# Performance work log

Measured on AMD Instinct MI355X. Metric: run time of the kernel, lower is better.

The kernel has to match this reference:

```python
import jax, jax.numpy as jnp
import numpy as np

N_E = 8192
E_DIM = 256
BETA = 0.25


def setup_inputs() -> dict:
    key = jax.random.key(0)
    k1, k2 = jax.random.split(key)
    z = jax.random.normal(k1, (16, E_DIM, 32, 32), dtype=jnp.float32)
    # matches torch init: uniform(-1/n_e, 1/n_e)
    emb_w = jax.random.uniform(k2, (N_E, E_DIM), dtype=jnp.float32,
                               minval=-1.0 / N_E, maxval=1.0 / N_E)
    return {"z": z, "emb_w": emb_w}


def reference(z, emb_w):
    B, C, H, W = z.shape
    zt = jnp.transpose(z, (0, 2, 3, 1))          # b h w c
    zf = zt.reshape(-1, C)                        # [N, e_dim]
    # d[n, k] = ||zf_n||^2 + ||e_k||^2 - 2 zf_n . e_k
    d = (jnp.sum(zf * zf, axis=1, keepdims=True)
         + jnp.sum(emb_w * emb_w, axis=1)
         - 2.0 * jnp.einsum('bd,nd->bn', zf, emb_w))
    idx = jnp.argmin(d, axis=1)                   # [N]
    z_q = emb_w[idx].reshape(zt.shape)            # b h w c
    sg = jax.lax.stop_gradient
    # legacy=True loss
    loss = jnp.mean((sg(z_q) - zt) ** 2) + BETA * jnp.mean((z_q - sg(zt)) ** 2)
    # straight-through estimator
    z_q_st = zt + sg(z_q - zt)
    z_q_out = jnp.transpose(z_q_st, (0, 3, 1, 2))  # b c h w
    return z_q_out, loss, idx.reshape(B, H, W)
```

## Files before the change

### kernel.cpp

```cpp
#include <hip/hip_runtime.h>
#include <math.h>

typedef unsigned int uint;
typedef unsigned short ushort;
typedef unsigned long long u64;
typedef __attribute__((ext_vector_type(8))) short short8;
typedef __attribute__((ext_vector_type(4))) float f32x4;

#define WS_ZT   0ull
#define WS_ZPK  16777216ull
#define WS_EPK  25165824ull
#define WS_SUMZ 29360128ull
#define WS_GMAX 29425664ull
#define WS_CMAX 46202880ull
#define WS_BEST 50397184ull
#define WS_LOSS 50528256ull

#define DOT_MARGIN 1.5e-4f

__device__ __forceinline__ ushort f2bf(float f) {
  uint b = __float_as_uint(f);
  b += 0x7fffu + ((b >> 16) & 1u);
  return (ushort)(b >> 16);
}
__device__ __forceinline__ uint ford(float f) {
  uint b = __float_as_uint(f);
  return (b & 0x80000000u) ? ~b : (b | 0x80000000u);
}
__device__ __forceinline__ void gload_lds16(const void* g, void* l) {
  __builtin_amdgcn_global_load_lds(
      (const __attribute__((address_space(1))) unsigned int*)g,
      (__attribute__((address_space(3))) unsigned int*)l, 16, 0, 0);
}

__global__ __launch_bounds__(256) void prep_all(const float* __restrict__ z,
                                                const float* __restrict__ emb,
                                                float* __restrict__ zt,
                                                ushort* __restrict__ zpk,
                                                ushort* __restrict__ epk,
                                                float* __restrict__ sumz) {
  __shared__ float tile[64][65];
  const int bidg = blockIdx.x;
  const int t = threadIdx.x;
  if (bidg < 1024) {
    const int bid = bidg;
    const int kt = bid & 3, hwt = (bid >> 2) & 15, b = bid >> 6;
    const int lane = t & 63, grp = t >> 6;
    const float* src = z + b * 262144 + (kt * 64) * 1024 + hwt * 64;
    for (int kk = grp; kk < 64; kk += 4)
      tile[kk][lane] = src[kk * 1024 + lane];
    __syncthreads();
    for (int rr = grp; rr < 64; rr += 4) {
      const int n = b * 1024 + hwt * 64 + rr;
      zt[n * 256 + kt * 64 + lane] = tile[lane][rr];
    }
    for (int u = t; u < 512; u += 256) {
      const int n_loc = u & 63, kg = u >> 6;
      const int n = b * 1024 + hwt * 64 + n_loc;
      const int k0 = kt * 64 + kg * 8;
      short8 s;
#pragma unroll
      for (int j = 0; j < 8; ++j) s[j] = (short)f2bf(tile[kg * 8 + j][n_loc]);
      *(short8*)(zpk + (size_t)(n >> 4) * 4096 + (k0 >> 5) * 512 +
                 ((k0 >> 3) & 3) * 128 + (n & 15) * 8) = s;
    }
  } else if (bidg < 2048) {
    const int u = (bidg - 1024) * 256 + t;
    const int c = u >> 5, k0 = (u & 31) * 8;
    const float4 v0 = *(const float4*)(emb + c * 256 + k0);
    const float4 v1 = *(const float4*)(emb + c * 256 + k0 + 4);
    short8 s;
    s[0] = (short)f2bf(v0.x); s[1] = (short)f2bf(v0.y);
    s[2] = (short)f2bf(v0.z); s[3] = (short)f2bf(v0.w);
    s[4] = (short)f2bf(v1.x); s[5] = (short)f2bf(v1.y);
    s[6] = (short)f2bf(v1.z); s[7] = (short)f2bf(v1.w);
    *(short8*)(epk + (size_t)(c >> 4) * 4096 + (k0 >> 5) * 512 +
               ((k0 >> 3) & 3) * 128 + (c & 15) * 8) = s;
  } else {
    const int n = ((bidg - 2048) << 8) + t;
    const int b = n >> 10, hw = n & 1023;
    const float* zb = z + b * 262144 + hw;
    float s = 0.f;
#pragma unroll 8
    for (int c = 0; c < 256; ++c) { const float v = zb[c << 10]; s += v * v; }
    sumz[n] = s;
  }
}

__global__ __launch_bounds__(256) void gemm_screen(const ushort* __restrict__ zpk,
                                                   const ushort* __restrict__ epk,
                                                   uint* __restrict__ gmax16,
                                                   ushort* __restrict__ cmax,
                                                   int boff) {
  __shared__ ushort Cs[16384];
  const int t = threadIdx.x;
  const int w = t >> 6, lane = t & 63;
  const int bid = blockIdx.x + boff;
  const int x = bid & 7, y = bid >> 3;
  const int yyv = y & 15;
  const int colb = yyv * 8 + x;
  const int rowg = y >> 4;
  const int n0 = rowg << 10;
  const int m16 = lane & 15, q = lane >> 4;

#pragma unroll
  for (int f2 = 0; f2 < 8; ++f2) {
    const int f = w * 8 + f2;
    gload_lds16(epk + (size_t)colb * 16384 + f * 512 + lane * 8, (char*)Cs + f * 1024);
  }

  const ushort* zw = zpk + ((size_t)(n0 >> 4) + w * 4) * 4096 + lane * 8;

  short8 zf[32][4];
#pragma unroll
  for (int v = 0; v < 3; ++v)
#pragma unroll
    for (int jr = 0; jr < 4; ++jr)
      zf[v][jr] = *(const short8*)(zw + ((size_t)((v >> 3) * 16 + jr)) * 4096 +
                                   (v & 7) * 512);
  __syncthreads();

#pragma unroll
  for (int strip = 0; strip < 4; ++strip) {
    const int rbase = n0 + strip * 256 + w * 64;
    f32x4 acc[4][4];
#pragma unroll
    for (int i = 0; i < 4; ++i)
#pragma unroll
      for (int j = 0; j < 4; ++j) acc[i][j] = {0.f, 0.f, 0.f, 0.f};

#pragma unroll
    for (int s32 = 0; s32 < 8; ++s32) {
      const int v = strip * 8 + s32;
      if (v + 3 < 32) {
        const int u = v + 3;
#pragma unroll
        for (int jr = 0; jr < 4; ++jr)
          zf[u][jr] = *(const short8*)(zw + ((size_t)((u >> 3) * 16 + jr)) * 4096 +
                                       (u & 7) * 512);
      }
      short8 cv[4];
#pragma unroll
      for (int ic = 0; ic < 4; ++ic)
        cv[ic] = *(const short8*)&Cs[(size_t)(ic * 8 + s32) * 512 + lane * 8];
#pragma unroll
      for (int ic = 0; ic < 4; ++ic)
#pragma unroll
        for (int jr = 0; jr < 4; ++jr)
          acc[ic][jr] = __builtin_amdgcn_mfma_f32_16x16x32_bf16(cv[ic], zf[v][jr],
                                                                acc[ic][jr], 0, 0, 0);
    }

#pragma unroll
    for (int jr = 0; jr < 4; ++jr) {
      float g16[4];
      float pm = -INFINITY;
#pragma unroll
      for (int ic = 0; ic < 4; ++ic) {
        float m = fmaxf(fmaxf(acc[ic][jr][0], acc[ic][jr][1]),
                        fmaxf(acc[ic][jr][2], acc[ic][jr][3]));
        m = fmaxf(m, __shfl_xor(m, 16, 64));
        const float o = __shfl_xor(m, 32, 64);
        const float g = fmaxf(m, o);
        g16[ic] = g;
        pm = fmaxf(pm, g);
      }
      const int row = rbase + jr * 16 + m16;
      const uint pa = (uint)f2bf(g16[0]) | ((uint)f2bf(g16[1]) << 16);
      const uint pb = (uint)f2bf(g16[2]) | ((uint)f2bf(g16[3]) << 16);
      if (q < 2)
        gmax16[(size_t)row * 256 + x * 32 + yyv * 2 + q] = (q == 0) ? pa : pb;
      if (q == 2)
        cmax[(size_t)row * 128 + x * 16 + yyv] = f2bf(pm);
    }
  }
}

__global__ __launch_bounds__(256) void select_rescore(const uint* __restrict__ gmax16,
                                                      const ushort* __restrict__ cmax,
                                                      const float* __restrict__ zt,
                                                      const float* __restrict__ emb,
                                                      const float* __restrict__ sumz,
                                                      u64* __restrict__ best) {
  const int t = threadIdx.x, w = t >> 6, lane = t & 63;
  const int n = (blockIdx.x << 2) + w;
  __shared__ float zrow[4][256];
  __shared__ ushort cands[4][32];
  ((float4*)zrow[w])[lane] = ((const float4*)(zt + (size_t)n * 256))[lane];

  const uint cu = ((const uint*)cmax)[(size_t)n * 64 + lane];
  const float c0 = __uint_as_float(cu << 16);
  const float c1 = __uint_as_float(cu & 0xffff0000u);
  float m = fmaxf(c0, c1);
#pragma unroll
  for (int off = 1; off < 64; off <<= 1) m = fmaxf(m, __shfl_xor(m, off, 64));
  const float thr = m - DOT_MARGIN;

  u64 m0 = __ballot(c0 >= thr);
  u64 m1 = __ballot(c1 >= thr);
  int nc = 0;
  while (m0 | m1) {
    int colp;
    if (m0) { const int s = __ffsll(m0) - 1; m0 &= m0 - 1; colp = s * 2; }
    else    { const int s = __ffsll(m1) - 1; m1 &= m1 - 1; colp = s * 2 + 1; }
    const int xx = colp >> 4, yy = colp & 15;
    const uint ua = gmax16[(size_t)n * 256 + xx * 32 + yy * 2];
    const uint ub = gmax16[(size_t)n * 256 + xx * 32 + yy * 2 + 1];
    const int gb = (yy * 8 + xx) * 4;
    const float f0 = __uint_as_float(ua << 16);
    const float f1 = __uint_as_float(ua & 0xffff0000u);
    const float f2 = __uint_as_float(ub << 16);
    const float f3 = __uint_as_float(ub & 0xffff0000u);
    if (f0 >= thr && nc < 32) { cands[w][nc] = (ushort)(gb + 0); ++nc; }
    if (f1 >= thr && nc < 32) { cands[w][nc] = (ushort)(gb + 1); ++nc; }
    if (f2 >= thr && nc < 32) { cands[w][nc] = (ushort)(gb + 2); ++nc; }
    if (f3 >= thr && nc < 32) { cands[w][nc] = (ushort)(gb + 3); ++nc; }
  }

  const int K = nc;
  const float sz = sumz[n];
  u64 bk = ~0ull;
  for (int id = lane; id < K * 16; id += 64) {
    const int g = cands[w][id >> 4];
    const int c = (g >> 2) * 64 + (g & 3) * 16 + (id & 15);
    const float4* ea = (const float4*)(emb + c * 256);
    const float4* za = (const float4*)zrow[w];
    float sdot = 0.f, se = 0.f;
#pragma unroll 8
    for (int k = 0; k < 64; ++k) {
      const float4 a = za[k], e = ea[k];
      sdot = fmaf(a.x, e.x, sdot); sdot = fmaf(a.y, e.y, sdot);
      sdot = fmaf(a.z, e.z, sdot); sdot = fmaf(a.w, e.w, sdot);
      se = fmaf(e.x, e.x, se); se = fmaf(e.y, e.y, se);
      se = fmaf(e.z, e.z, se); se = fmaf(e.w, e.w, se);
    }
    const float d = (sz + se) - 2.f * sdot;
    const u64 key = ((u64)ford(d) << 32) | (uint)c;
    if (key < bk) bk = key;
  }
#pragma unroll
  for (int off = 1; off < 64; off <<= 1) {
    const u64 o = (((u64)(uint)__shfl_xor((int)(bk >> 32), off, 64)) << 32) |
                  (uint)__shfl_xor((int)(bk & 0xffffffffu), off, 64);
    if (o < bk) bk = o;
  }
  if (lane == 0) best[n] = bk;
}

__global__ __launch_bounds__(256) void gather_kernel(const float* __restrict__ z,
                                                     const float* __restrict__ emb,
                                                     const u64* __restrict__ best,
                                                     float* __restrict__ out,
                                                     double* __restrict__ loss_acc,
                                                     uint* __restrict__ done) {
  const int t = threadIdx.x;
  const int n0 = blockIdx.x << 6;
  const int n = n0 + (t & 63);
  const int idx = (int)(best[n] & 0xffffffffull);
  const int b_i = n >> 10, hw = n & 1023;
  const int c0 = t >> 6;
  const float* zb = z + b_i * 262144 + hw;
  float* ob = out + b_i * 262144 + hw;
  const float* eb = emb + idx * 256;
  float lsum = 0.f;
#pragma unroll 4
  for (int c = c0; c < 256; c += 4) {
    const float ev = eb[c];
    const float zv = zb[c << 10];
    ob[c << 10] = ev;
    const float d = ev - zv;
    lsum += d * d;
  }
  if (c0 == 0) out[4194305 + n] = (float)idx;
#pragma unroll
  for (int off = 32; off; off >>= 1) lsum += __shfl_down(lsum, off, 64);
  __shared__ double wsum[4];
  if ((t & 63) == 0) wsum[t >> 6] = (double)lsum;
  __syncthreads();
  if (t == 0) {
    atomicAdd(loss_acc, wsum[0] + wsum[1] + wsum[2] + wsum[3]);
    __threadfence();
    if (atomicAdd(done, 1u) == 255u) {
      __threadfence();
      out[4194304] = (float)(1.25 * (*(volatile double*)loss_acc) / 4194304.0);
    }
  }
}

extern "C" void kernel_launch(void* const* d_in, const int* in_sizes, int n_in,
                              void* d_out, int out_size, void* d_ws, size_t ws_size,
                              hipStream_t stream) {
  const float* z = (const float*)d_in[0];
  const float* emb = (const float*)d_in[1];
  float* out = (float*)d_out;
  char* ws = (char*)d_ws;
  float* zt = (float*)(ws + WS_ZT);
  ushort* zpk = (ushort*)(ws + WS_ZPK);
  ushort* epk = (ushort*)(ws + WS_EPK);
  float* sumz = (float*)(ws + WS_SUMZ);
  uint* gmax16 = (uint*)(ws + WS_GMAX);
  ushort* cmax = (ushort*)(ws + WS_CMAX);
  u64* best = (u64*)(ws + WS_BEST);
  double* loss_acc = (double*)(ws + WS_LOSS);
  uint* done = (uint*)(ws + WS_LOSS + 8);

  hipMemsetAsync(ws + WS_LOSS, 0, 16, stream);
  prep_all<<<2112, 256, 0, stream>>>(z, emb, zt, zpk, epk, sumz);
  gemm_screen<<<1024, 256, 0, stream>>>(zpk, epk, gmax16, cmax, 0);
  gemm_screen<<<1024, 256, 0, stream>>>(zpk, epk, gmax16, cmax, 1024);
  select_rescore<<<4096, 256, 0, stream>>>(gmax16, cmax, zt, emb, sumz, best);
  gather_kernel<<<256, 256, 0, stream>>>(z, emb, best, out, loss_acc, done);
}
```

Before: 265.1 us.

## Refine screening to 8-code groups and drop transposed fp32 z copy

The gemm screen now stores per-row maxima for groups of 8 codes instead of 16, so rescoring evaluates fewer candidate codes in exact fp32. The 16 MB transposed z copy is removed; select_rescore gathers each z row from the original strided layout instead. The best index is stored as a 32-bit uint. This trades a doubled gmax buffer write and strided z reads against less prep traffic and fewer fp32 dot products.

```diff
diff --git a/kernel.cpp b/kernel.cpp
--- a/kernel.cpp
+++ b/kernel.cpp
@@ -7,14 +7,13 @@
 typedef __attribute__((ext_vector_type(8))) short short8;
 typedef __attribute__((ext_vector_type(4))) float f32x4;
 
-#define WS_ZT   0ull
-#define WS_ZPK  16777216ull
-#define WS_EPK  25165824ull
-#define WS_SUMZ 29360128ull
-#define WS_GMAX 29425664ull
+#define WS_ZPK  0ull
+#define WS_EPK  8388608ull
+#define WS_SUMZ 12582912ull
+#define WS_GMAX 12648448ull
 #define WS_CMAX 46202880ull
 #define WS_BEST 50397184ull
-#define WS_LOSS 50528256ull
+#define WS_LOSS 50462720ull
 
 #define DOT_MARGIN 1.5e-4f
 
@@ -35,7 +34,6 @@
 
 __global__ __launch_bounds__(256) void prep_all(const float* __restrict__ z,
                                                 const float* __restrict__ emb,
-                                                float* __restrict__ zt,
                                                 ushort* __restrict__ zpk,
                                                 ushort* __restrict__ epk,
                                                 float* __restrict__ sumz) {
@@ -50,10 +48,6 @@
     for (int kk = grp; kk < 64; kk += 4)
       tile[kk][lane] = src[kk * 1024 + lane];
     __syncthreads();
-    for (int rr = grp; rr < 64; rr += 4) {
-      const int n = b * 1024 + hwt * 64 + rr;
-      zt[n * 256 + kt * 64 + lane] = tile[lane][rr];
-    }
     for (int u = t; u < 512; u += 256) {
       const int n_loc = u & 63, kg = u >> 6;
       const int n = b * 1024 + hwt * 64 + n_loc;
@@ -89,7 +83,7 @@
 
 __global__ __launch_bounds__(256) void gemm_screen(const ushort* __restrict__ zpk,
                                                    const ushort* __restrict__ epk,
-                                                   uint* __restrict__ gmax16,
+                                                   uint* __restrict__ gmax,
                                                    ushort* __restrict__ cmax,
                                                    int boff) {
   __shared__ ushort Cs[16384];
@@ -102,6 +96,7 @@
   const int rowg = y >> 4;
   const int n0 = rowg << 10;
   const int m16 = lane & 15, q = lane >> 4;
+  const int cix = x * 64 + yyv * 4 + q;
 
 #pragma unroll
   for (int f2 = 0; f2 < 8; ++f2) {
@@ -153,7 +148,7 @@
 
 #pragma unroll
     for (int jr = 0; jr < 4; ++jr) {
-      float g16[4];
+      uint pk[4];
       float pm = -INFINITY;
 #pragma unroll
       for (int ic = 0; ic < 4; ++ic) {
@@ -161,32 +156,33 @@
                         fmaxf(acc[ic][jr][2], acc[ic][jr][3]));
         m = fmaxf(m, __shfl_xor(m, 16, 64));
         const float o = __shfl_xor(m, 32, 64);
-        const float g = fmaxf(m, o);
-        g16[ic] = g;
-        pm = fmaxf(pm, g);
+        pm = fmaxf(pm, fmaxf(m, o));
+        const float glo = (q & 2) ? o : m;
+        const float ghi = (q & 2) ? m : o;
+        pk[ic] = (uint)f2bf(glo) | ((uint)f2bf(ghi) << 16);
       }
+      const uint sv = (q == 0) ? pk[0] : (q == 1) ? pk[1] : (q == 2) ? pk[2] : pk[3];
       const int row = rbase + jr * 16 + m16;
-      const uint pa = (uint)f2bf(g16[0]) | ((uint)f2bf(g16[1]) << 16);
-      const uint pb = (uint)f2bf(g16[2]) | ((uint)f2bf(g16[3]) << 16);
-      if (q < 2)
-        gmax16[(size_t)row * 256 + x * 32 + yyv * 2 + q] = (q == 0) ? pa : pb;
-      if (q == 2)
-        cmax[(size_t)row * 128 + x * 16 + yyv] = f2bf(pm);
-    }
-  }
-}
-
-__global__ __launch_bounds__(256) void select_rescore(const uint* __restrict__ gmax16,
+      gmax[(size_t)row * 512 + cix] = sv;
+      if (q == 0) cmax[(size_t)row * 128 + x * 16 + yyv] = f2bf(pm);
+    }
+  }
+}
+
+__global__ __launch_bounds__(256) void select_rescore(const uint* __restrict__ gmax,
                                                       const ushort* __restrict__ cmax,
-                                                      const float* __restrict__ zt,
+                                                      const float* __restrict__ z,
                                                       const float* __restrict__ emb,
                                                       const float* __restrict__ sumz,
-                                                      u64* __restrict__ best) {
+                                                      uint* __restrict__ bestI) {
   const int t = threadIdx.x, w = t >> 6, lane = t & 63;
   const int n = (blockIdx.x << 2) + w;
   __shared__ float zrow[4][256];
-  __shared__ ushort cands[4][32];
-  ((float4*)zrow[w])[lane] = ((const float4*)(zt + (size_t)n * 256))[lane];
+  __shared__ ushort hits[4][64];
+  const int b_i = n >> 10, hw = n & 1023;
+  const float* zb = z + b_i * 262144 + hw;
+#pragma unroll
+  for (int j = 0; j < 4; ++j) zrow[w][lane + j * 64] = zb[(lane + j * 64) << 10];
 
   const uint cu = ((const uint*)cmax)[(size_t)n * 64 + lane];
   const float c0 = __uint_as_float(cu << 16);
@@ -198,31 +194,29 @@
 
   u64 m0 = __ballot(c0 >= thr);
   u64 m1 = __ballot(c1 >= thr);
-  int nc = 0;
+  int nh = 0;
   while (m0 | m1) {
-    int colp;
-    if (m0) { const int s = __ffsll(m0) - 1; m0 &= m0 - 1; colp = s * 2; }
-    else    { const int s = __ffsll(m1) - 1; m1 &= m1 - 1; colp = s * 2 + 1; }
-    const int xx = colp >> 4, yy = colp & 15;
-    const uint ua = gmax16[(size_t)n * 256 + xx * 32 + yy * 2];
-    const uint ub = gmax16[(size_t)n * 256 + xx * 32 + yy * 2 + 1];
-    const int gb = (yy * 8 + xx) * 4;
-    const float f0 = __uint_as_float(ua << 16);
-    const float f1 = __uint_as_float(ua & 0xffff0000u);
-    const float f2 = __uint_as_float(ub << 16);
-    const float f3 = __uint_as_float(ub & 0xffff0000u);
-    if (f0 >= thr && nc < 32) { cands[w][nc] = (ushort)(gb + 0); ++nc; }
-    if (f1 >= thr && nc < 32) { cands[w][nc] = (ushort)(gb + 1); ++nc; }
-    if (f2 >= thr && nc < 32) { cands[w][nc] = (ushort)(gb + 2); ++nc; }
-    if (f3 >= thr && nc < 32) { cands[w][nc] = (ushort)(gb + 3); ++nc; }
-  }
-
-  const int K = nc;
+    int p;
+    if (m0) { const int s = (int)__builtin_ctzll(m0); m0 &= m0 - 1; p = s * 2; }
+    else    { const int s = (int)__builtin_ctzll(m1); m1 &= m1 - 1; p = s * 2 + 1; }
+    const int xx = p >> 4, yy = p & 15;
+    const int cb = (yy * 8 + xx) * 64;
+    const uint4 fw = *(const uint4*)(gmax + (size_t)n * 512 + xx * 64 + yy * 4);
+    const uint fq[4] = {fw.x, fw.y, fw.z, fw.w};
+#pragma unroll
+    for (int qq = 0; qq < 4; ++qq) {
+      if (__uint_as_float(fq[qq] << 16) >= thr && nh < 64)
+        hits[w][nh++] = (ushort)(cb + qq * 16);
+      if (__uint_as_float(fq[qq] & 0xffff0000u) >= thr && nh < 64)
+        hits[w][nh++] = (ushort)(cb + qq * 16 + 8);
+    }
+  }
+  __threadfence_block();
+  const int K = nh;
   const float sz = sumz[n];
   u64 bk = ~0ull;
-  for (int id = lane; id < K * 16; id += 64) {
-    const int g = cands[w][id >> 4];
-    const int c = (g >> 2) * 64 + (g & 3) * 16 + (id & 15);
+  for (int id = lane; id < K * 8; id += 64) {
+    const int c = hits[w][id >> 3] + (id & 7);
     const float4* ea = (const float4*)(emb + c * 256);
     const float4* za = (const float4*)zrow[w];
     float sdot = 0.f, se = 0.f;
@@ -244,19 +238,19 @@
                   (uint)__shfl_xor((int)(bk & 0xffffffffu), off, 64);
     if (o < bk) bk = o;
   }
-  if (lane == 0) best[n] = bk;
+  if (lane == 0) bestI[n] = (uint)(bk & 0xffffffffu);
 }
 
 __global__ __launch_bounds__(256) void gather_kernel(const float* __restrict__ z,
                                                      const float* __restrict__ emb,
-                                                     const u64* __restrict__ best,
+                                                     const uint* __restrict__ bestI,
                                                      float* __restrict__ out,
                                                      double* __restrict__ loss_acc,
                                                      uint* __restrict__ done) {
   const int t = threadIdx.x;
   const int n0 = blockIdx.x << 6;
   const int n = n0 + (t & 63);
-  const int idx = (int)(best[n] & 0xffffffffull);
+  const int idx = (int)bestI[n];
   const int b_i = n >> 10, hw = n & 1023;
   const int c0 = t >> 6;
   const float* zb = z + b_i * 262144 + hw;
@@ -294,20 +288,19 @@
   const float* emb = (const float*)d_in[1];
   float* out = (float*)d_out;
   char* ws = (char*)d_ws;
-  float* zt = (float*)(ws + WS_ZT);
   ushort* zpk = (ushort*)(ws + WS_ZPK);
   ushort* epk = (ushort*)(ws + WS_EPK);
   float* sumz = (float*)(ws + WS_SUMZ);
-  uint* gmax16 = (uint*)(ws + WS_GMAX);
+  uint* gmax = (uint*)(ws + WS_GMAX);
   ushort* cmax = (ushort*)(ws + WS_CMAX);
-  u64* best = (u64*)(ws + WS_BEST);
+  uint* bestI = (uint*)(ws + WS_BEST);
   double* loss_acc = (double*)(ws + WS_LOSS);
   uint* done = (uint*)(ws + WS_LOSS + 8);
 
   hipMemsetAsync(ws + WS_LOSS, 0, 16, stream);
-  prep_all<<<2112, 256, 0, stream>>>(z, emb, zt, zpk, epk, sumz);
-  gemm_screen<<<1024, 256, 0, stream>>>(zpk, epk, gmax16, cmax, 0);
-  gemm_screen<<<1024, 256, 0, stream>>>(zpk, epk, gmax16, cmax, 1024);
-  select_rescore<<<4096, 256, 0, stream>>>(gmax16, cmax, zt, emb, sumz, best);
-  gather_kernel<<<256, 256, 0, stream>>>(z, emb, best, out, loss_acc, done);
-}
+  prep_all<<<2112, 256, 0, stream>>>(z, emb, zpk, epk, sumz);
+  gemm_screen<<<1024, 256, 0, stream>>>(zpk, epk, gmax, cmax, 0);
+  gemm_screen<<<1024, 256, 0, stream>>>(zpk, epk, gmax, cmax, 1024);
+  select_rescore<<<4096, 256, 0, stream>>>(gmax, cmax, z, emb, sumz, bestI);
+  gather_kernel<<<256, 256, 0, stream>>>(z, emb, bestI, out, loss_acc, done);
+}
```

New measurement: 258.5 us. -2.5%, faster.
